# Kernel tuning notes

Hardware: AMD Instinct MI355X
Metric: run time of the kernel (lower is better)

Reference implementation:

```python
import jax, jax.numpy as jnp
import numpy as np

# Grid config from init_kwargs
VX, VY = 0.1, 0.1
XMIN, YMIN, ZMIN, XMAX, YMAX, ZMAX = 0.0, -25.6, -3.0, 51.2, 25.6, 3.0
H = int(round((XMAX - XMIN) / VX))  # 512
W = int(round((YMAX - YMIN) / VY))  # 512
SIGMA = 1.5   # gaussian std in voxel units
R = 3         # splat window radius -> 7x7 kernel


def _pose0to1(pose0, pose1):
    # ego-motion: pose1^{-1} @ pose0, per batch element
    return jnp.linalg.inv(pose1) @ pose0


def _transform(xyz, pose):
    # xyz: [B,N,3], pose: [B,4,4] -> xyz @ R^T + t
    Rm = pose[:, :3, :3]
    t = pose[:, :3, 3]
    return jnp.einsum('bnd,bed->bne', xyz, Rm) + t[:, None, :]


def _voxelize(xyz):
    # continuous voxel coords + integer pillar indices + in-range mask
    px = (xyz[..., 0] - XMIN) / VX
    py = (xyz[..., 1] - YMIN) / VY
    ix = jnp.floor(px).astype(jnp.int32)
    iy = jnp.floor(py).astype(jnp.int32)
    valid = (ix >= 0) & (ix < H) & (iy >= 0) & (iy < W) & \
            (xyz[..., 2] >= ZMIN) & (xyz[..., 2] < ZMAX)
    return px, py, ix, iy, valid


def _gauss_heatmap(px, py, ix, iy, valid):
    # Splat a gaussian (max-composited) around every valid radar pillar.
    B, M = px.shape
    offs = jnp.arange(-R, R + 1)
    dx, dy = jnp.meshgrid(offs, offs, indexing='ij')      # [K,K]
    gx = ix[:, :, None, None] + dx                        # [B,M,K,K]
    gy = iy[:, :, None, None] + dy
    cellx = gx.astype(px.dtype) + 0.5
    celly = gy.astype(py.dtype) + 0.5
    d2 = (cellx - px[:, :, None, None]) ** 2 + (celly - py[:, :, None, None]) ** 2
    val = jnp.exp(-d2 / (2.0 * SIGMA * SIGMA))
    inb = (gx >= 0) & (gx < H) & (gy >= 0) & (gy < W) & valid[:, :, None, None]
    bidx = jnp.arange(B, dtype=jnp.int32)[:, None, None, None]
    flat = jnp.where(inb, bidx * (H * W) + gx * W + gy, B * H * W)  # dummy seg for invalid
    heat = jax.ops.segment_max(val.reshape(-1), flat.reshape(-1),
                               num_segments=B * H * W + 1)
    heat = jnp.maximum(heat[:B * H * W], 0.0).reshape(B, H, W)
    return heat


def _gather(heat, ix, iy, valid):
    # per-point gaussian score = heatmap at the point's pillar
    B = heat.shape[0]
    hf = heat.reshape(B, -1)
    idx = jnp.clip(ix, 0, H - 1) * W + jnp.clip(iy, 0, W - 1)
    s = jnp.take_along_axis(hf, idx, axis=1)
    return jnp.where(valid, s, 0.0)


def _forward(pc0, pc1, radar_pc0, radar_pc1, pose0, pose1):
    # pose computed under no_grad in the original -> stop_gradient
    pose_0to1 = jax.lax.stop_gradient(_pose0to1(pose0, pose1))
    tpc0 = _transform(pc0, pose_0to1)
    trad0_xyz = _transform(radar_pc0[..., :3], pose_0to1)
    # dynamic pillar voxelization (BEV coords)
    _, _, l0x, l0y, l0v = _voxelize(tpc0)
    _, _, l1x, l1y, l1v = _voxelize(pc1)
    r0px, r0py, r0x, r0y, r0v = _voxelize(trad0_xyz)
    r1px, r1py, r1x, r1y, r1v = _voxelize(radar_pc1[..., :3])
    # gaussian maps from radar pillars, scored for lidar + radar points
    heat0 = _gauss_heatmap(r0px, r0py, r0x, r0y, r0v)
    heat1 = _gauss_heatmap(r1px, r1py, r1x, r1y, r1v)
    lidar0 = _gather(heat0, l0x, l0y, l0v)   # [B,N]
    radar0 = _gather(heat0, r0x, r0y, r0v)   # [B,M]
    lidar1 = _gather(heat1, l1x, l1y, l1v)
    radar1 = _gather(heat1, r1x, r1y, r1v)
    return jnp.concatenate([lidar0, radar0, lidar1, radar1], axis=1)


def setup_inputs() -> dict:
    key = jax.random.key(0)
    ks = jax.random.split(key, 8)
    B, N, M = 8, 262144, 8192
    lo = jnp.array([XMIN, YMIN, ZMIN], dtype=jnp.float32)
    hi = jnp.array([XMAX, YMAX, ZMAX], dtype=jnp.float32)
    pc0 = jax.random.uniform(ks[0], (B, N, 3), dtype=jnp.float32) * (hi - lo) + lo
    pc1 = jax.random.uniform(ks[1], (B, N, 3), dtype=jnp.float32) * (hi - lo) + lo
    rxyz0 = jax.random.uniform(ks[2], (B, M, 3), dtype=jnp.float32) * (hi - lo) + lo
    rxyz1 = jax.random.uniform(ks[3], (B, M, 3), dtype=jnp.float32) * (hi - lo) + lo
    radar_pc0 = jnp.concatenate([rxyz0, jax.random.normal(ks[4], (B, M, 3), dtype=jnp.float32)], axis=-1)
    radar_pc1 = jnp.concatenate([rxyz1, jax.random.normal(ks[5], (B, M, 3), dtype=jnp.float32)], axis=-1)

    def mk_pose(k):
        t = jax.random.uniform(k, (B, 3), minval=-0.5, maxval=0.5, dtype=jnp.float32)
        eye = jnp.tile(jnp.eye(4, dtype=jnp.float32)[None], (B, 1, 1))
        return eye.at[:, :3, 3].set(t)

    pose0 = mk_pose(ks[6])
    pose1 = mk_pose(ks[7])
    return {"pc0": pc0, "pc1": pc1, "radar_pc0": radar_pc0,
            "radar_pc1": radar_pc1, "pose0": pose0, "pose1": pose1}


def reference(pc0, pc1, radar_pc0, radar_pc1, pose0, pose1):
    return _forward(pc0, pc1, radar_pc0, radar_pc1, pose0, pose1)
```

## Files before the change

kernel.cpp:

```cpp
#include <hip/hip_runtime.h>
#include <math.h>

#define GH 512
#define GW 512
#define GHW (GH * GW)
#define RR 3
#define TS 64
#define TSHIFT 6
#define TPB 8
#define NTILES (TPB * TPB)
#define CAP 1024


__global__ void pose_init_kernel(const float* __restrict__ pose0,
                                 const float* __restrict__ pose1,
                                 float* __restrict__ pose_out,
                                 int* __restrict__ counts,
                                 int B, int nbins) {
    int t = threadIdx.x;
    for (int i = t; i < nbins; i += 64) counts[i] = 0;
    if (t >= B) return;
    const float* P1 = pose1 + t * 16;
    const float* P0 = pose0 + t * 16;
    double a00 = P1[0], a01 = P1[1], a02 = P1[2],  t1x = P1[3];
    double a10 = P1[4], a11 = P1[5], a12 = P1[6],  t1y = P1[7];
    double a20 = P1[8], a21 = P1[9], a22 = P1[10], t1z = P1[11];
    double c00 = a11 * a22 - a12 * a21;
    double c01 = a12 * a20 - a10 * a22;
    double c02 = a10 * a21 - a11 * a20;
    double det = a00 * c00 + a01 * c01 + a02 * c02;
    double id = 1.0 / det;
    double r00 = c00 * id;
    double r01 = (a02 * a21 - a01 * a22) * id;
    double r02 = (a01 * a12 - a02 * a11) * id;
    double r10 = c01 * id;
    double r11 = (a00 * a22 - a02 * a20) * id;
    double r12 = (a02 * a10 - a00 * a12) * id;
    double r20 = c02 * id;
    double r21 = (a01 * a20 - a00 * a21) * id;
    double r22 = (a00 * a11 - a01 * a10) * id;

    double b00 = P0[0], b01 = P0[1], b02 = P0[2],  t0x = P0[3];
    double b10 = P0[4], b11 = P0[5], b12 = P0[6],  t0y = P0[7];
    double b20 = P0[8], b21 = P0[9], b22 = P0[10], t0z = P0[11];
    double dx = t0x - t1x, dy = t0y - t1y, dz = t0z - t1z;

    float* O = pose_out + t * 16;
    O[0]  = (float)(r00 * b00 + r01 * b10 + r02 * b20);
    O[1]  = (float)(r00 * b01 + r01 * b11 + r02 * b21);
    O[2]  = (float)(r00 * b02 + r01 * b12 + r02 * b22);
    O[3]  = (float)(r00 * dx + r01 * dy + r02 * dz);
    O[4]  = (float)(r10 * b00 + r11 * b10 + r12 * b20);
    O[5]  = (float)(r10 * b01 + r11 * b11 + r12 * b21);
    O[6]  = (float)(r10 * b02 + r11 * b12 + r12 * b22);
    O[7]  = (float)(r10 * dx + r11 * dy + r12 * dz);
    O[8]  = (float)(r20 * b00 + r21 * b10 + r22 * b20);
    O[9]  = (float)(r20 * b01 + r21 * b11 + r22 * b21);
    O[10] = (float)(r20 * b02 + r21 * b12 + r22 * b22);
    O[11] = (float)(r20 * dx + r21 * dy + r22 * dz);
    O[12] = 0.0f; O[13] = 0.0f; O[14] = 0.0f; O[15] = 1.0f;
}

__device__ __forceinline__ void voxelize_xyz(float x, float y, float z,
                                             const float* __restrict__ T,
                                             float& px, float& py,
                                             int& ix, int& iy, bool& valid) {
    if (T) {
        float nx = T[0] * x + T[1] * y + T[2] * z + T[3];
        float ny = T[4] * x + T[5] * y + T[6] * z + T[7];
        float nz = T[8] * x + T[9] * y + T[10] * z + T[11];
        x = nx; y = ny; z = nz;
    }
    px = (x - 0.0f) * 10.0f;
    py = (y - (-25.6f)) * 10.0f;
    ix = (int)floorf(px);
    iy = (int)floorf(py);
    valid = (ix >= 0) & (ix < GH) & (iy >= 0) & (iy < GW) &
            (z >= -3.0f) & (z < 3.0f);
}

__device__ __forceinline__ void voxelize_f32(const float* __restrict__ p,
                                             const float* __restrict__ T,
                                             float& px, float& py,
                                             int& ix, int& iy, bool& valid) {
    voxelize_xyz(p[0], p[1], p[2], T, px, py, ix, iy, valid);
}

__global__ __launch_bounds__(256)
void scatter_direct_kernel(const float* __restrict__ radar0,
                           const float* __restrict__ radar1,
                           const float* __restrict__ pose,
                           int* __restrict__ counts,
                           unsigned int* __restrict__ entries,
                           int B, int M) {
    int t = blockIdx.x * 256 + threadIdx.x;
    int BM = B * M;
    if (t >= 2 * BM) return;
    int map = t / BM;
    int rem = t - map * BM;
    int b = rem / M;
    const float* radar = map ? radar1 : radar0;
    const float* T = map ? nullptr : (pose + b * 16);
    const float* p = radar + (size_t)rem * 6;
    float px, py; int ix, iy; bool valid;
    voxelize_f32(p, T, px, py, ix, iy, valid);
    if (!valid) return;
    int txlo = max(ix - RR, 0) >> TSHIFT, txhi = min(ix + RR, GH - 1) >> TSHIFT;
    int tylo = max(iy - RR, 0) >> TSHIFT, tyhi = min(iy + RR, GW - 1) >> TSHIFT;
    int binbase = (map * B + b) * NTILES;
    for (int tx = txlo; tx <= txhi; tx++)
        for (int ty = tylo; ty <= tyhi; ty++) {
            int bin = binbase + tx * TPB + ty;
            int slot = atomicAdd(&counts[bin], 1);
            if (slot < CAP) entries[(size_t)bin * CAP + slot] = (unsigned int)t;
        }
}

__global__ __launch_bounds__(256)
void tile_splat_kernel(const float* __restrict__ radar0,
                       const float* __restrict__ radar1,
                       const float* __restrict__ pose,
                       const int* __restrict__ counts,
                       const unsigned int* __restrict__ entries,
                       float* __restrict__ heat0,
                       float* __restrict__ heat1,
                       int B, int M) {
    __shared__ int tile[TS * TS];
    __shared__ float spx[CAP];
    __shared__ float spy[CAP];
    const int tid = threadIdx.x;
    const int tileIdx = blockIdx.x;
    const int b = blockIdx.y;
    const int map = blockIdx.z;
    const int BM = B * M;
    const int tx0 = (tileIdx >> 3) << TSHIFT;
    const int ty0 = (tileIdx & 7) << TSHIFT;

    for (int c = tid; c < TS * TS; c += 256) tile[c] = 0;

    const int bin = (map * B + b) * NTILES + tileIdx;
    int n = counts[bin];
    if (n > CAP) n = CAP;
    const size_t base = (size_t)bin * CAP;
    const float* radar = map ? radar1 : radar0;
    const float* T = map ? nullptr : (pose + b * 16);

    for (int i = tid; i < n; i += 256) {
        unsigned int e = entries[base + i];
        int rem = (int)e - map * BM;
        const float* p = radar + (size_t)rem * 6;
        float px, py; int ix, iy; bool valid;
        voxelize_f32(p, T, px, py, ix, iy, valid);
        spx[i] = px;
        spy[i] = py;
    }
    __syncthreads();

    const int total = n * 49;
    for (int t = tid; t < total; t += 256) {
        int pi = t / 49;
        int c = t - pi * 49;
        float px = spx[pi];
        float py = spy[pi];
        int ix = (int)floorf(px);
        int iy = (int)floorf(py);
        int dx = c / 7 - RR;
        int dy = c - (c / 7) * 7 - RR;
        int gx = ix + dx, gy = iy + dy;
        if (gx < tx0 || gx >= tx0 + TS || gy < ty0 || gy >= ty0 + TS) continue;
        float ddx = ((float)gx + 0.5f) - px;
        float ddy = ((float)gy + 0.5f) - py;
        float d2 = ddx * ddx + ddy * ddy;
        float val = expf(-d2 / 4.5f);
        atomicMax(&tile[(gx - tx0) * TS + (gy - ty0)], __float_as_int(val));
    }
    __syncthreads();

    float* heat = map ? heat1 : heat0;
    float* hb = heat + (size_t)b * GHW;
    for (int c = tid; c < TS * TS; c += 256) {
        int lx = c >> TSHIFT, ly = c & (TS - 1);
        hb[(tx0 + lx) * GW + (ty0 + ly)] = __int_as_float(tile[c]);
    }
}

__global__ __launch_bounds__(256)
void gather_fused_kernel(const float* __restrict__ pc0,
                         const float* __restrict__ pc1,
                         const float* __restrict__ radar0,
                         const float* __restrict__ radar1,
                         const float* __restrict__ pose,
                         const float* __restrict__ heat0,
                         const float* __restrict__ heat1,
                         float* __restrict__ out,
                         int N, int M) {
    const int row_len = 2 * N + 2 * M;
    const int b = blockIdx.x;
    const int base = blockIdx.y * 2048 + threadIdx.x;
    const float* hb0 = heat0 + (size_t)b * GHW;
    const float* hb1 = heat1 + (size_t)b * GHW;
    const float* Tb = pose + b * 16;

    float xs[8], ys[8], zs[8];
    const float* Ts[8];
    const float* hbs[8];
    bool live[8];

    #pragma unroll
    for (int k = 0; k < 8; k++) {
        int r = base + k * 256;
        live[k] = (r < row_len);
        if (!live[k]) continue;
        const float* p;
        const float* T = nullptr;
        const float* hb;
        if (r < N) {
            p = pc0 + ((size_t)b * N + r) * 3;
            T = Tb;
            hb = hb0;
        } else if (r < N + M) {
            p = radar0 + ((size_t)b * M + (r - N)) * 6;
            T = Tb;
            hb = hb0;
        } else if (r < 2 * N + M) {
            p = pc1 + ((size_t)b * N + (r - N - M)) * 3;
            hb = hb1;
        } else {
            p = radar1 + ((size_t)b * M + (r - 2 * N - M)) * 6;
            hb = hb1;
        }
        xs[k] = __builtin_nontemporal_load(p + 0);
        ys[k] = __builtin_nontemporal_load(p + 1);
        zs[k] = __builtin_nontemporal_load(p + 2);
        Ts[k] = T;
        hbs[k] = hb;
    }

    float v[8];
    #pragma unroll
    for (int k = 0; k < 8; k++) {
        if (!live[k]) continue;
        float px, py; int ix, iy; bool valid;
        voxelize_xyz(xs[k], ys[k], zs[k], Ts[k], px, py, ix, iy, valid);
        v[k] = 0.0f;
        if (valid) v[k] = hbs[k][ix * GW + iy];
    }

    #pragma unroll
    for (int k = 0; k < 8; k++) {
        if (!live[k]) continue;
        int r = base + k * 256;
        __builtin_nontemporal_store(v[k], out + (size_t)b * row_len + r);
    }
}

extern "C" void kernel_launch(void* const* d_in, const int* in_sizes, int n_in,
                              void* d_out, int out_size, void* d_ws, size_t ws_size,
                              hipStream_t stream) {
    const float* pc0      = (const float*)d_in[0];
    const float* pc1      = (const float*)d_in[1];
    const float* radar0   = (const float*)d_in[2];
    const float* radar1   = (const float*)d_in[3];
    const float* pose0    = (const float*)d_in[4];
    const float* pose1    = (const float*)d_in[5];
    float* out = (float*)d_out;

    int B = in_sizes[4] / 16;
    int N = in_sizes[0] / (B * 3);
    int M = in_sizes[2] / (B * 6);
    int row_len = 2 * N + 2 * M;
    int BM = B * M;
    int nbins = 2 * B * NTILES;

    float* heat0   = (float*)d_ws;
    float* heat1   = heat0 + (size_t)B * GHW;
    float* pose_ws = heat1 + (size_t)B * GHW;
    int*   counts  = (int*)(pose_ws + B * 16);
    unsigned int* entries = (unsigned int*)(counts + nbins);

    pose_init_kernel<<<1, 64, 0, stream>>>(pose0, pose1, pose_ws, counts, B, nbins);

    int pts_blocks = (2 * BM + 255) / 256;
    scatter_direct_kernel<<<pts_blocks, 256, 0, stream>>>(
        radar0, radar1, pose_ws, counts, entries, B, M);

    dim3 sgrid(NTILES, B, 2);
    tile_splat_kernel<<<sgrid, 256, 0, stream>>>(
        radar0, radar1, pose_ws, counts, entries, heat0, heat1, B, M);

    dim3 ggrid(B, (row_len + 2047) / 2048);
    gather_fused_kernel<<<ggrid, 256, 0, stream>>>(
        pc0, pc1, radar0, radar1, pose_ws, heat0, heat1, out, N, M);
}
```

Baseline: 164.6 us.

## Fuse binning and splat into one heat kernel with per-tile point scan

Removes the pose-init and scatter/binning kernels. Each tile block now scans every radar point of its batch, filters those whose splat window touches the tile into shared memory, and recomputes the ego pose inverse itself. The gather kernel also computes the pose locally, and the heatmap write-out uses float4 stores. This saves two launches and the global atomics and entry-list traffic, at the cost of every tile block re-reading all M points, a redundant scan that grows with M times the 64 tiles.

```diff
diff --git a/kernel.cpp b/kernel.cpp
--- a/kernel.cpp
+++ b/kernel.cpp
@@ -12,16 +12,9 @@
 #define CAP 1024
 
 
-__global__ void pose_init_kernel(const float* __restrict__ pose0,
-                                 const float* __restrict__ pose1,
-                                 float* __restrict__ pose_out,
-                                 int* __restrict__ counts,
-                                 int B, int nbins) {
-    int t = threadIdx.x;
-    for (int i = t; i < nbins; i += 64) counts[i] = 0;
-    if (t >= B) return;
-    const float* P1 = pose1 + t * 16;
-    const float* P0 = pose0 + t * 16;
+__device__ __forceinline__ void compute_pose(const float* __restrict__ P0,
+                                             const float* __restrict__ P1,
+                                             float* __restrict__ T) {
     double a00 = P1[0], a01 = P1[1], a02 = P1[2],  t1x = P1[3];
     double a10 = P1[4], a11 = P1[5], a12 = P1[6],  t1y = P1[7];
     double a20 = P1[8], a21 = P1[9], a22 = P1[10], t1z = P1[11];
@@ -45,20 +38,18 @@
     double b20 = P0[8], b21 = P0[9], b22 = P0[10], t0z = P0[11];
     double dx = t0x - t1x, dy = t0y - t1y, dz = t0z - t1z;
 
-    float* O = pose_out + t * 16;
-    O[0]  = (float)(r00 * b00 + r01 * b10 + r02 * b20);
-    O[1]  = (float)(r00 * b01 + r01 * b11 + r02 * b21);
-    O[2]  = (float)(r00 * b02 + r01 * b12 + r02 * b22);
-    O[3]  = (float)(r00 * dx + r01 * dy + r02 * dz);
-    O[4]  = (float)(r10 * b00 + r11 * b10 + r12 * b20);
-    O[5]  = (float)(r10 * b01 + r11 * b11 + r12 * b21);
-    O[6]  = (float)(r10 * b02 + r11 * b12 + r12 * b22);
-    O[7]  = (float)(r10 * dx + r11 * dy + r12 * dz);
-    O[8]  = (float)(r20 * b00 + r21 * b10 + r22 * b20);
-    O[9]  = (float)(r20 * b01 + r21 * b11 + r22 * b21);
-    O[10] = (float)(r20 * b02 + r21 * b12 + r22 * b22);
-    O[11] = (float)(r20 * dx + r21 * dy + r22 * dz);
-    O[12] = 0.0f; O[13] = 0.0f; O[14] = 0.0f; O[15] = 1.0f;
+    T[0]  = (float)(r00 * b00 + r01 * b10 + r02 * b20);
+    T[1]  = (float)(r00 * b01 + r01 * b11 + r02 * b21);
+    T[2]  = (float)(r00 * b02 + r01 * b12 + r02 * b22);
+    T[3]  = (float)(r00 * dx + r01 * dy + r02 * dz);
+    T[4]  = (float)(r10 * b00 + r11 * b10 + r12 * b20);
+    T[5]  = (float)(r10 * b01 + r11 * b11 + r12 * b21);
+    T[6]  = (float)(r10 * b02 + r11 * b12 + r12 * b22);
+    T[7]  = (float)(r10 * dx + r11 * dy + r12 * dz);
+    T[8]  = (float)(r20 * b00 + r21 * b10 + r22 * b20);
+    T[9]  = (float)(r20 * b01 + r21 * b11 + r22 * b21);
+    T[10] = (float)(r20 * b02 + r21 * b12 + r22 * b22);
+    T[11] = (float)(r20 * dx + r21 * dy + r22 * dz);
 }
 
 __device__ __forceinline__ void voxelize_xyz(float x, float y, float z,
@@ -79,83 +70,53 @@
             (z >= -3.0f) & (z < 3.0f);
 }
 
-__device__ __forceinline__ void voxelize_f32(const float* __restrict__ p,
-                                             const float* __restrict__ T,
-                                             float& px, float& py,
-                                             int& ix, int& iy, bool& valid) {
-    voxelize_xyz(p[0], p[1], p[2], T, px, py, ix, iy, valid);
-}
-
 __global__ __launch_bounds__(256)
-void scatter_direct_kernel(const float* __restrict__ radar0,
-                           const float* __restrict__ radar1,
-                           const float* __restrict__ pose,
-                           int* __restrict__ counts,
-                           unsigned int* __restrict__ entries,
-                           int B, int M) {
-    int t = blockIdx.x * 256 + threadIdx.x;
-    int BM = B * M;
-    if (t >= 2 * BM) return;
-    int map = t / BM;
-    int rem = t - map * BM;
-    int b = rem / M;
-    const float* radar = map ? radar1 : radar0;
-    const float* T = map ? nullptr : (pose + b * 16);
-    const float* p = radar + (size_t)rem * 6;
-    float px, py; int ix, iy; bool valid;
-    voxelize_f32(p, T, px, py, ix, iy, valid);
-    if (!valid) return;
-    int txlo = max(ix - RR, 0) >> TSHIFT, txhi = min(ix + RR, GH - 1) >> TSHIFT;
-    int tylo = max(iy - RR, 0) >> TSHIFT, tyhi = min(iy + RR, GW - 1) >> TSHIFT;
-    int binbase = (map * B + b) * NTILES;
-    for (int tx = txlo; tx <= txhi; tx++)
-        for (int ty = tylo; ty <= tyhi; ty++) {
-            int bin = binbase + tx * TPB + ty;
-            int slot = atomicAdd(&counts[bin], 1);
-            if (slot < CAP) entries[(size_t)bin * CAP + slot] = (unsigned int)t;
-        }
-}
-
-__global__ __launch_bounds__(256)
-void tile_splat_kernel(const float* __restrict__ radar0,
-                       const float* __restrict__ radar1,
-                       const float* __restrict__ pose,
-                       const int* __restrict__ counts,
-                       const unsigned int* __restrict__ entries,
-                       float* __restrict__ heat0,
-                       float* __restrict__ heat1,
-                       int B, int M) {
+void heat_kernel(const float* __restrict__ radar0,
+                 const float* __restrict__ radar1,
+                 const float* __restrict__ pose0,
+                 const float* __restrict__ pose1,
+                 float* __restrict__ heat0,
+                 float* __restrict__ heat1,
+                 int B, int M) {
     __shared__ int tile[TS * TS];
     __shared__ float spx[CAP];
     __shared__ float spy[CAP];
+    __shared__ float Tsh[12];
+    __shared__ int sn;
+
     const int tid = threadIdx.x;
-    const int tileIdx = blockIdx.x;
-    const int b = blockIdx.y;
-    const int map = blockIdx.z;
-    const int BM = B * M;
+    const int blk = blockIdx.x;
+    const int b = blk % B;
+    const int map = (blk / B) & 1;
+    const int tileIdx = blk / (2 * B);
     const int tx0 = (tileIdx >> 3) << TSHIFT;
     const int ty0 = (tileIdx & 7) << TSHIFT;
 
+    if (tid == 0) {
+        sn = 0;
+        if (map == 0) compute_pose(pose0 + b * 16, pose1 + b * 16, Tsh);
+    }
     for (int c = tid; c < TS * TS; c += 256) tile[c] = 0;
-
-    const int bin = (map * B + b) * NTILES + tileIdx;
-    int n = counts[bin];
-    if (n > CAP) n = CAP;
-    const size_t base = (size_t)bin * CAP;
+    __syncthreads();
+
     const float* radar = map ? radar1 : radar0;
-    const float* T = map ? nullptr : (pose + b * 16);
-
-    for (int i = tid; i < n; i += 256) {
-        unsigned int e = entries[base + i];
-        int rem = (int)e - map * BM;
-        const float* p = radar + (size_t)rem * 6;
+    const float* T = map ? nullptr : Tsh;
+    const float* pb = radar + (size_t)b * M * 6;
+
+    for (int i = tid; i < M; i += 256) {
+        const float* p = pb + (size_t)i * 6;
+        float x = p[0], y = p[1], z = p[2];
         float px, py; int ix, iy; bool valid;
-        voxelize_f32(p, T, px, py, ix, iy, valid);
-        spx[i] = px;
-        spy[i] = py;
-    }
-    __syncthreads();
-
+        voxelize_xyz(x, y, z, T, px, py, ix, iy, valid);
+        if (!valid) continue;
+        if (ix < tx0 - RR || ix > tx0 + TS - 1 + RR ||
+            iy < ty0 - RR || iy > ty0 + TS - 1 + RR) continue;
+        int slot = atomicAdd(&sn, 1);
+        if (slot < CAP) { spx[slot] = px; spy[slot] = py; }
+    }
+    __syncthreads();
+
+    int n = sn; if (n > CAP) n = CAP;
     const int total = n * 49;
     for (int t = tid; t < total; t += 256) {
         int pi = t / 49;
@@ -178,9 +139,15 @@
 
     float* heat = map ? heat1 : heat0;
     float* hb = heat + (size_t)b * GHW;
-    for (int c = tid; c < TS * TS; c += 256) {
-        int lx = c >> TSHIFT, ly = c & (TS - 1);
-        hb[(tx0 + lx) * GW + (ty0 + ly)] = __int_as_float(tile[c]);
+    for (int c4 = tid * 4; c4 < TS * TS; c4 += 1024) {
+        int lx = c4 >> TSHIFT, ly = c4 & (TS - 1);
+        int4 iv = *reinterpret_cast<const int4*>(&tile[c4]);
+        float4 fv;
+        fv.x = __int_as_float(iv.x);
+        fv.y = __int_as_float(iv.y);
+        fv.z = __int_as_float(iv.z);
+        fv.w = __int_as_float(iv.w);
+        *reinterpret_cast<float4*>(hb + (size_t)(tx0 + lx) * GW + (ty0 + ly)) = fv;
     }
 }
 
@@ -189,17 +156,23 @@
                          const float* __restrict__ pc1,
                          const float* __restrict__ radar0,
                          const float* __restrict__ radar1,
-                         const float* __restrict__ pose,
+                         const float* __restrict__ pose0,
+                         const float* __restrict__ pose1,
                          const float* __restrict__ heat0,
                          const float* __restrict__ heat1,
                          float* __restrict__ out,
                          int N, int M) {
+    __shared__ float Tsh[12];
     const int row_len = 2 * N + 2 * M;
     const int b = blockIdx.x;
     const int base = blockIdx.y * 2048 + threadIdx.x;
+
+    if (threadIdx.x == 0) compute_pose(pose0 + b * 16, pose1 + b * 16, Tsh);
+    __syncthreads();
+
     const float* hb0 = heat0 + (size_t)b * GHW;
     const float* hb1 = heat1 + (size_t)b * GHW;
-    const float* Tb = pose + b * 16;
+    const float* Tb = Tsh;
 
     float xs[8], ys[8], zs[8];
     const float* Ts[8];
@@ -269,26 +242,15 @@
     int N = in_sizes[0] / (B * 3);
     int M = in_sizes[2] / (B * 6);
     int row_len = 2 * N + 2 * M;
-    int BM = B * M;
-    int nbins = 2 * B * NTILES;
-
-    float* heat0   = (float*)d_ws;
-    float* heat1   = heat0 + (size_t)B * GHW;
-    float* pose_ws = heat1 + (size_t)B * GHW;
-    int*   counts  = (int*)(pose_ws + B * 16);
-    unsigned int* entries = (unsigned int*)(counts + nbins);
-
-    pose_init_kernel<<<1, 64, 0, stream>>>(pose0, pose1, pose_ws, counts, B, nbins);
-
-    int pts_blocks = (2 * BM + 255) / 256;
-    scatter_direct_kernel<<<pts_blocks, 256, 0, stream>>>(
-        radar0, radar1, pose_ws, counts, entries, B, M);
-
-    dim3 sgrid(NTILES, B, 2);
-    tile_splat_kernel<<<sgrid, 256, 0, stream>>>(
-        radar0, radar1, pose_ws, counts, entries, heat0, heat1, B, M);
+
+    float* heat0 = (float*)d_ws;
+    float* heat1 = heat0 + (size_t)B * GHW;
+
+    int nblk = 2 * B * NTILES;
+    heat_kernel<<<nblk, 256, 0, stream>>>(
+        radar0, radar1, pose0, pose1, heat0, heat1, B, M);
 
     dim3 ggrid(B, (row_len + 2047) / 2048);
     gather_fused_kernel<<<ggrid, 256, 0, stream>>>(
-        pc0, pc1, radar0, radar1, pose_ws, heat0, heat1, out, N, M);
-}
+        pc0, pc1, radar0, radar1, pose0, pose1, heat0, heat1, out, N, M);
+}
```

After: 158.9 us. -3.4%, faster.
